# Optimization experiments

Hardware: AMD Instinct MI355X
Metric: run time of the kernel (lower is better)

Reference implementation:

```python
import jax, jax.numpy as jnp
import numpy as np

LAMBDA = 0.95   # cfg.lambda_decay
ETA = 0.5       # cfg.eta
EPS_REL = 1e-6  # cfg.epsilon (relative-error denom)
S_INNER = 3     # cfg.inner_steps
LN_EPS = 1e-5   # torch LayerNorm default eps

T, B, D_G, D_H = 48, 48, 256, 512


def setup_inputs() -> dict:
    key = jax.random.key(0)
    ks = jax.random.split(key, 5)
    # scale weights ~ kaiming/xavier so the recurrence is well-behaved
    return {
        "z_seq": jax.random.normal(ks[0], (T, B, D_G), jnp.float32),
        "clean_vec": jax.random.normal(ks[1], (B, D_G), jnp.float32),
        "W_h": jax.random.normal(ks[2], (D_H, D_H), jnp.float32) * (2.0 / D_H) ** 0.5,
        "W_g": jax.random.normal(ks[3], (D_H, D_G), jnp.float32) * (1.0 / D_G) ** 0.5,
        "b_h": jnp.zeros((D_H,), jnp.float32),
        "gamma": jnp.ones((D_H,), jnp.float32),
        "beta": jnp.zeros((D_H,), jnp.float32),
        "W_head": jax.random.normal(ks[4], (D_G, D_H), jnp.float32) * (1.0 / D_H) ** 0.5,
        "b_head": jnp.zeros((D_G,), jnp.float32),
    }


def _layernorm(x, gamma, beta):
    mu = jnp.mean(x, axis=-1, keepdims=True)
    var = jnp.mean(jnp.square(x - mu), axis=-1, keepdims=True)
    return (x - mu) * jax.lax.rsqrt(var + LN_EPS) * gamma + beta


def reference(z_seq, clean_vec, W_h, W_g, b_h, gamma, beta, W_head, b_head):
    Bsz = clean_vec.shape[0]
    d_h = W_h.shape[0]
    h0 = jnp.zeros((Bsz, d_h), z_seq.dtype)
    A0 = jnp.zeros((Bsz, d_h, d_h), z_seq.dtype)

    def step(carry, z_t):
        h_prev, A = carry
        base = h_prev @ W_h.T + z_t @ W_g.T + b_h          # (B, d_h)
        h = jax.nn.relu(_layernorm(base, gamma, beta))
        for _ in range(S_INNER):                            # inner fast-weight settling
            add_Ah = jnp.einsum('bij,bj->bi', A, h)         # bmm(A, h)
            h = jax.nn.relu(_layernorm(base + add_Ah, gamma, beta))
        A = LAMBDA * A + ETA * jnp.einsum('bi,bj->bij', h, h)  # Hebbian outer-product update
        return (h, A), None

    (h, A), _ = jax.lax.scan(step, (h0, A0), z_seq)

    pred_vec = h @ W_head.T + b_head                        # (B, d_g)
    pred_norm = pred_vec / (jnp.linalg.norm(pred_vec, axis=1, keepdims=True) + 1e-6)
    clean_norm = clean_vec / (jnp.linalg.norm(clean_vec, axis=1, keepdims=True) + 1e-6)
    sq_err = jnp.sum(jnp.square(pred_vec - clean_vec), axis=1)
    denom = jnp.sum(jnp.square(clean_vec), axis=1) + EPS_REL
    loss = jnp.mean(sq_err / denom)
    acc = jnp.mean(jnp.sum(pred_norm * clean_norm, axis=1))
    return loss, acc
```

## Files before the change

### kernel.cpp

```cpp
#include <hip/hip_runtime.h>

#define T_STEPS 48
#define BATCH   48
#define DG      256
#define DH      512
#define S_INNER 3
#define HDSTRIDE 260

typedef _Float16 hf2 __attribute__((ext_vector_type(2)));

__device__ __forceinline__ hf2 bch(unsigned u) { return __builtin_bit_cast(hf2, u); }
__device__ __forceinline__ unsigned pkh(_Float16 a, _Float16 b) {
  hf2 v{a, b}; return __builtin_bit_cast(unsigned, v);
}
__device__ __forceinline__ float fdot2u(unsigned a, unsigned b, float c) {
#if __has_builtin(__builtin_amdgcn_fdot2)
  return __builtin_amdgcn_fdot2(bch(a), bch(b), c, false);
#else
  hf2 x = bch(a), y = bch(b);
  return fmaf((float)x.x, (float)y.x, fmaf((float)x.y, (float)y.y, c));
#endif
}
__device__ __forceinline__ float wave_reduce_sum(float v) {
  #pragma unroll
  for (int off = 32; off > 0; off >>= 1) v += __shfl_xor(v, off, 64);
  return v;
}
template <int CTRL>
__device__ __forceinline__ float dpp_add(float v) {
  int t = __builtin_amdgcn_update_dpp(0, __float_as_int(v), CTRL, 0xf, 0xf, true);
  return v + __int_as_float(t);
}
template <int CTRL>
__device__ __forceinline__ float dpp_mov(float v) {
  return __int_as_float(
      __builtin_amdgcn_update_dpp(0, __float_as_int(v), CTRL, 0xf, 0xf, true));
}
__device__ __forceinline__ float wave64_sum63(float v) {
  v = dpp_add<0xB1>(v);
  v = dpp_add<0x4E>(v);
  v = dpp_add<0x141>(v);
  v = dpp_add<0x140>(v);
  v = dpp_add<0x142>(v);
  v = dpp_add<0x143>(v);
  return v;
}
__device__ __forceinline__ float row16_sum(float v) {
  v = dpp_add<0xB1>(v);
  v = dpp_add<0x4E>(v);
  v = dpp_add<0x141>(v);
  v = dpp_add<0x140>(v);
  return v;
}

__global__ __launch_bounds__(256)
void pack_whq(const float* __restrict__ W, uint2* __restrict__ Wq) {
  int idx = blockIdx.x * 256 + threadIdx.x;
  int j = idx & (DH - 1), q = idx >> 9;
  float w0 = W[(size_t)(4 * q + 0) * DH + j];
  float w1 = W[(size_t)(4 * q + 1) * DH + j];
  float w2 = W[(size_t)(4 * q + 2) * DH + j];
  float w3 = W[(size_t)(4 * q + 3) * DH + j];
  uint2 o;
  o.x = pkh((_Float16)w0, (_Float16)w1);
  o.y = pkh((_Float16)w2, (_Float16)w3);
  Wq[(size_t)j * 128 + q] = o;
}

__global__ __launch_bounds__(256)
void transpose_k(const float* __restrict__ in, float* __restrict__ out, int R, int C) {
  __shared__ float tile[32][33];
  int c0 = blockIdx.x * 32, r0 = blockIdx.y * 32;
  int tx = threadIdx.x & 31, ty = threadIdx.x >> 5;
  #pragma unroll
  for (int k = 0; k < 32; k += 8)
    tile[ty + k][tx] = in[(size_t)(r0 + ty + k) * C + (c0 + tx)];
  __syncthreads();
  #pragma unroll
  for (int k = 0; k < 32; k += 8)
    out[(size_t)(c0 + ty + k) * R + (r0 + tx)] = tile[tx][ty + k];
}

__global__ __launch_bounds__(DH, 2)
void zg_kernel(const float* __restrict__ z, const float* __restrict__ WgT,
               float* __restrict__ ZG) {
  const int row0 = blockIdx.x * 8;
  const int tid = threadIdx.x;
  __shared__ __align__(16) float zl[8][DG];
  for (int i = tid; i < 8 * (DG / 4); i += DH) {
    int r = i >> 6, c = i & 63;
    ((float4*)zl[r])[c] = ((const float4*)(z + (size_t)(row0 + r) * DG))[c];
  }
  __syncthreads();
  float acc[8] = {0.f, 0.f, 0.f, 0.f, 0.f, 0.f, 0.f, 0.f};
  for (int j = 0; j < DG; j += 4) {
    float w0 = WgT[(size_t)(j + 0) * DH + tid];
    float w1 = WgT[(size_t)(j + 1) * DH + tid];
    float w2 = WgT[(size_t)(j + 2) * DH + tid];
    float w3 = WgT[(size_t)(j + 3) * DH + tid];
    #pragma unroll
    for (int r = 0; r < 8; ++r) {
      float4 zz = ((const float4*)zl[r])[j >> 2];
      acc[r] = fmaf(w0, zz.x, acc[r]);
      acc[r] = fmaf(w1, zz.y, acc[r]);
      acc[r] = fmaf(w2, zz.z, acc[r]);
      acc[r] = fmaf(w3, zz.w, acc[r]);
    }
  }
  #pragma unroll
  for (int r = 0; r < 8; ++r)
    ZG[(size_t)(row0 + r) * DH + tid] = acc[r];
}

#define HCASE(s) case (2*(s)): hreg[(s)] = hb; break; \
                 case (2*(s)+1): hreg[(s)] |= (hb << 16); break;

__global__ __launch_bounds__(1024, 4)
void rnn_main(const float* __restrict__ ZG, const uint2* __restrict__ Whq,
              const float* __restrict__ bh, const float* __restrict__ gamma,
              const float* __restrict__ beta, const float* __restrict__ W_head,
              const float* __restrict__ b_head, const float* __restrict__ clean,
              float* __restrict__ outbuf) {
  const int b = blockIdx.x;
  const int tid  = threadIdx.x;
  const int lane = tid & 63;
  const int wv   = tid >> 6;
  const int dim  = tid;
  const bool lower = tid < DH;
  const int q     = tid & 127;
  const int slice = tid >> 7;
  const bool isdot = tid < 768;
  const int dst = tid >> 4;
  const int dj  = tid & 15;

  __shared__ __align__(16) unsigned histd[T_STEPS * HDSTRIDE];
  __shared__ __align__(16) float    pm[8 * DH];
  __shared__ __align__(16) uint2    APr[8 * 64];
  __shared__ __align__(16) unsigned h2cur[256];
  __shared__ __align__(16) unsigned cbufh2[24];
  __shared__ __align__(16) float    hcur[DH];
  __shared__ __align__(16) float    pred[DG];
  __shared__ float2 red[8];
  __shared__ float  red4[64];
  __shared__ int    wcntp[8];
  __shared__ float  lampow[T_STEPS];

  float g_i = 0.f, be_i = 0.f, bh_i = 0.f;
  if (lower) { g_i = gamma[dim]; be_i = beta[dim]; bh_i = bh[dim]; }
  if (tid == 0) {
    float pw = 0.5f;
    for (int k = 0; k < T_STEPS; ++k) { lampow[k] = pw; pw *= 0.95f; }
  }
  unsigned hreg[24];
  #pragma unroll
  for (int k = 0; k < 24; ++k) hreg[k] = 0u;

  const char* Wb = (const char*)Whq;
  const unsigned q8 = (unsigned)(q << 3);
  __syncthreads();

  for (int t = 0; t < T_STEPS; ++t) {
    float zg = lower ? ZG[((size_t)t * BATCH + b) * DH + dim] : 0.f;

    uint4 hr0, hr1, hr2, hr3;
    if (isdot) {
      const unsigned* rp = histd + dst * HDSTRIDE + 4 * dj;
      hr0 = *(const uint4*)(rp + 0);
      hr1 = *(const uint4*)(rp + 64);
      hr2 = *(const uint4*)(rp + 128);
      hr3 = *(const uint4*)(rp + 192);
    } else {
      hr0 = hr1 = hr2 = hr3 = make_uint4(0u, 0u, 0u, 0u);
    }

    {
      hf2 ma0{}, ma1{}, mc0{}, mc1{};
      if (t > 0) {
        const int n = wcntp[slice];
        if (n > 0) {
          const uint4* ap4 = (const uint4*)(APr + slice * 64);
          uint4 E0 = ap4[0], E1 = ap4[1];
          uint2 w0 = *(const uint2*)(Wb + (E0.x + q8));
          uint2 w1 = *(const uint2*)(Wb + (E0.z + q8));
          uint2 w2 = *(const uint2*)(Wb + (E1.x + q8));
          uint2 w3 = *(const uint2*)(Wb + (E1.z + q8));
          for (int m = 4; m < n; m += 4) {
            uint4 F0 = ap4[m >> 1], F1 = ap4[(m >> 1) + 1];
            uint2 v0 = *(const uint2*)(Wb + (F0.x + q8));
            uint2 v1 = *(const uint2*)(Wb + (F0.z + q8));
            uint2 v2 = *(const uint2*)(Wb + (F1.x + q8));
            uint2 v3 = *(const uint2*)(Wb + (F1.z + q8));
            ma0 += bch(w0.x) * bch(E0.y); mc0 += bch(w0.y) * bch(E0.y);
            ma1 += bch(w1.x) * bch(E0.w); mc1 += bch(w1.y) * bch(E0.w);
            ma0 += bch(w2.x) * bch(E1.y); mc0 += bch(w2.y) * bch(E1.y);
            ma1 += bch(w3.x) * bch(E1.w); mc1 += bch(w3.y) * bch(E1.w);
            E0 = F0; E1 = F1;
            w0 = v0; w1 = v1; w2 = v2; w3 = v3;
          }
          ma0 += bch(w0.x) * bch(E0.y); mc0 += bch(w0.y) * bch(E0.y);
          ma1 += bch(w1.x) * bch(E0.w); mc1 += bch(w1.y) * bch(E0.w);
          ma0 += bch(w2.x) * bch(E1.y); mc0 += bch(w2.y) * bch(E1.y);
          ma1 += bch(w3.x) * bch(E1.w); mc1 += bch(w3.y) * bch(E1.w);
        }
      }
      float4 s4;
      s4.x = (float)ma0.x + (float)ma1.x; s4.y = (float)ma0.y + (float)ma1.y;
      s4.z = (float)mc0.x + (float)mc1.x; s4.w = (float)mc0.y + (float)mc1.y;
      ((float4*)(pm + slice * DH))[q] = s4;
    }
    __syncthreads();

    float base_i = 0.f;
    if (lower) {
      base_i = bh_i + zg;
      if (t > 0) {
        float ps = 0.f;
        #pragma unroll
        for (int sl = 0; sl < 8; ++sl) ps += pm[sl * DH + dim];
        base_i += ps;
      }
    }

    for (int inr = 0; inr <= S_INNER; ++inr) {
      float x = 0.f;
      if (lower) {
        float Ah = 0.f;
        if (inr > 0 && t > 0) {
          const uint4* cbp = (const uint4*)cbufh2;
          uint4 c0 = cbp[0], c1 = cbp[1], c2 = cbp[2];
          uint4 c3 = cbp[3], c4 = cbp[4], c5 = cbp[5];
          float A0 = 0.f, A1 = 0.f, A2 = 0.f, A3 = 0.f;
          A0 = fdot2u(hreg[0],  c0.x, A0); A1 = fdot2u(hreg[1],  c0.y, A1);
          A2 = fdot2u(hreg[2],  c0.z, A2); A3 = fdot2u(hreg[3],  c0.w, A3);
          A0 = fdot2u(hreg[4],  c1.x, A0); A1 = fdot2u(hreg[5],  c1.y, A1);
          A2 = fdot2u(hreg[6],  c1.z, A2); A3 = fdot2u(hreg[7],  c1.w, A3);
          A0 = fdot2u(hreg[8],  c2.x, A0); A1 = fdot2u(hreg[9],  c2.y, A1);
          A2 = fdot2u(hreg[10], c2.z, A2); A3 = fdot2u(hreg[11], c2.w, A3);
          A0 = fdot2u(hreg[12], c3.x, A0); A1 = fdot2u(hreg[13], c3.y, A1);
          A2 = fdot2u(hreg[14], c3.z, A2); A3 = fdot2u(hreg[15], c3.w, A3);
          A0 = fdot2u(hreg[16], c4.x, A0); A1 = fdot2u(hreg[17], c4.y, A1);
          A2 = fdot2u(hreg[18], c4.z, A2); A3 = fdot2u(hreg[19], c4.w, A3);
          A0 = fdot2u(hreg[20], c5.x, A0); A1 = fdot2u(hreg[21], c5.y, A1);
          A2 = fdot2u(hreg[22], c5.z, A2); A3 = fdot2u(hreg[23], c5.w, A3);
          Ah = (A0 + A1) + (A2 + A3);
        }
        x = base_i + Ah;
        float sa = wave64_sum63(x);
        float sb = wave64_sum63(x * x);
        if (lane == 63) red[wv] = make_float2(sa, sb);
      }
      __syncthreads();

      if (inr < S_INNER) {
        if (lower) {
          const float4* rr = (const float4*)red;
          float4 r0 = rr[0], r1 = rr[1], r2 = rr[2], r3 = rr[3];
          float s  = ((r0.x + r1.x) + (r2.x + r3.x)) + ((r0.z + r1.z) + (r2.z + r3.z));
          float s2 = ((r0.y + r1.y) + (r2.y + r3.y)) + ((r0.w + r1.w) + (r2.w + r3.w));
          const float inv = 1.f / (float)DH;
          float mu  = s * inv;
          float var = s2 * inv - mu * mu;
          float rstd = rsqrtf(var + 1e-5f);
          float h = fmaxf(fmaf((x - mu) * rstd, g_i, be_i), 0.f);
          float hn = dpp_mov<0xB1>(h);
          if (!(dim & 1)) h2cur[dim >> 1] = pkh((_Float16)h, (_Float16)hn);
        }
        __syncthreads();
        if (isdot) {
          const unsigned* hp = h2cur + 4 * dj;
          uint4 v0 = *(const uint4*)(hp + 0);
          uint4 v1 = *(const uint4*)(hp + 64);
          uint4 v2 = *(const uint4*)(hp + 128);
          uint4 v3 = *(const uint4*)(hp + 192);
          float a0 = 0.f, a1 = 0.f, a2 = 0.f, a3 = 0.f;
          a0 = fdot2u(hr0.x, v0.x, a0); a1 = fdot2u(hr0.y, v0.y, a1);
          a2 = fdot2u(hr0.z, v0.z, a2); a3 = fdot2u(hr0.w, v0.w, a3);
          a0 = fdot2u(hr1.x, v1.x, a0); a1 = fdot2u(hr1.y, v1.y, a1);
          a2 = fdot2u(hr1.z, v1.z, a2); a3 = fdot2u(hr1.w, v1.w, a3);
          a0 = fdot2u(hr2.x, v2.x, a0); a1 = fdot2u(hr2.y, v2.y, a1);
          a2 = fdot2u(hr2.z, v2.z, a2); a3 = fdot2u(hr2.w, v2.w, a3);
          a0 = fdot2u(hr3.x, v3.x, a0); a1 = fdot2u(hr3.y, v3.y, a1);
          a2 = fdot2u(hr3.z, v3.z, a2); a3 = fdot2u(hr3.w, v3.w, a3);
          float pd = row16_sum((a0 + a1) + (a2 + a3));
          float cc = (dst < t) ? pd * lampow[t - 1 - dst] : 0.f;
          if (dj == 0) {
            _Float16 ch = (_Float16)cc;
            ((unsigned short*)cbufh2)[dst] = __builtin_bit_cast(unsigned short, ch);
          }
        }
        __syncthreads();
      } else {
        if (lower) {
          const float4* rr = (const float4*)red;
          float4 r0 = rr[0], r1 = rr[1], r2 = rr[2], r3 = rr[3];
          float s  = ((r0.x + r1.x) + (r2.x + r3.x)) + ((r0.z + r1.z) + (r2.z + r3.z));
          float s2 = ((r0.y + r1.y) + (r2.y + r3.y)) + ((r0.w + r1.w) + (r2.w + r3.w));
          const float inv = 1.f / (float)DH;
          float mu  = s * inv;
          float var = s2 * inv - mu * mu;
          float rstd = rsqrtf(var + 1e-5f);
          float h = fmaxf(fmaf((x - mu) * rstd, g_i, be_i), 0.f);
          unsigned hb = (unsigned)__builtin_bit_cast(unsigned short, (_Float16)h);
          float hn = dpp_mov<0xB1>(h);
          if (!(dim & 1))
            histd[t * HDSTRIDE + (dim >> 1)] = pkh((_Float16)h, (_Float16)hn);
          switch (t) {
            HCASE(0)  HCASE(1)  HCASE(2)  HCASE(3)  HCASE(4)  HCASE(5)
            HCASE(6)  HCASE(7)  HCASE(8)  HCASE(9)  HCASE(10) HCASE(11)
            HCASE(12) HCASE(13) HCASE(14) HCASE(15) HCASE(16) HCASE(17)
            HCASE(18) HCASE(19) HCASE(20) HCASE(21) HCASE(22) HCASE(23)
          }
          if (t == T_STEPS - 1) hcur[dim] = h;
          unsigned long long mb = __ballot(h != 0.f);
          int myoff = __popcll(mb & ((1ull << lane) - 1ull));
          int wc  = __popcll(mb);
          int wcp = (wc + 3) & ~3;
          if (h != 0.f) {
            _Float16 hh = (_Float16)h;
            uint2 ent; ent.x = (unsigned)(dim << 10); ent.y = pkh(hh, hh);
            APr[wv * 64 + myoff] = ent;
          } else {
            int inact = lane - myoff;
            if (inact < wcp - wc) {
              uint2 zz; zz.x = 0u; zz.y = 0u;
              APr[wv * 64 + wc + inact] = zz;
            }
          }
          if (lane == 0) wcntp[wv] = wcp;
        }
        __syncthreads();
      }
    }
  }

  for (int r = wv; r < DG; r += 16) {
    const float4* w4  = (const float4*)(W_head + (size_t)r * DH);
    const float4* hc4 = (const float4*)hcur;
    float pdot = 0.f;
    #pragma unroll
    for (int kk = 0; kk < 2; ++kk) {
      float4 a4 = w4[lane + 64 * kk];
      float4 c4 = hc4[lane + 64 * kk];
      pdot += a4.x * c4.x + a4.y * c4.y + a4.z * c4.z + a4.w * c4.w;
    }
    pdot = wave_reduce_sum(pdot);
    if (lane == 0) pred[r] = pdot + b_head[r];
  }
  __syncthreads();

  float sq = 0.f, pc = 0.f, pp = 0.f, cc = 0.f;
  if (tid < DG) {
    float pv = pred[tid];
    float cv = clean[(size_t)b * DG + tid];
    float d = pv - cv;
    sq = d * d; pc = pv * cv; pp = pv * pv; cc = cv * cv;
  }
  #pragma unroll
  for (int off = 32; off > 0; off >>= 1) {
    sq += __shfl_xor(sq, off, 64);
    pc += __shfl_xor(pc, off, 64);
    pp += __shfl_xor(pp, off, 64);
    cc += __shfl_xor(cc, off, 64);
  }
  if (lane == 0) {
    red4[wv * 4 + 0] = sq; red4[wv * 4 + 1] = pc;
    red4[wv * 4 + 2] = pp; red4[wv * 4 + 3] = cc;
  }
  __syncthreads();
  if (tid == 0) {
    float Sq = 0.f, Pc = 0.f, Pp = 0.f, Cc = 0.f;
    #pragma unroll
    for (int w = 0; w < 16; ++w) {
      Sq += red4[w * 4 + 0]; Pc += red4[w * 4 + 1];
      Pp += red4[w * 4 + 2]; Cc += red4[w * 4 + 3];
    }
    outbuf[b]         = Sq / (Cc + 1e-6f);
    outbuf[BATCH + b] = Pc / ((sqrtf(Pp) + 1e-6f) * (sqrtf(Cc) + 1e-6f));
  }
}

__global__ __launch_bounds__(64)
void finalize_k(const float* __restrict__ outbuf, float* __restrict__ out) {
  int tid = threadIdx.x;
  float l = (tid < BATCH) ? outbuf[tid] : 0.f;
  float a = (tid < BATCH) ? outbuf[BATCH + tid] : 0.f;
  #pragma unroll
  for (int off = 32; off > 0; off >>= 1) {
    l += __shfl_xor(l, off, 64);
    a += __shfl_xor(a, off, 64);
  }
  if (tid == 0) {
    out[0] = l * (1.f / (float)BATCH);
    out[1] = a * (1.f / (float)BATCH);
  }
}

extern "C" void kernel_launch(void* const* d_in, const int* in_sizes, int n_in,
                              void* d_out, int out_size, void* d_ws, size_t ws_size,
                              hipStream_t stream) {
  (void)in_sizes; (void)n_in; (void)out_size; (void)ws_size;
  const float* z      = (const float*)d_in[0];
  const float* clean  = (const float*)d_in[1];
  const float* W_h    = (const float*)d_in[2];
  const float* W_g    = (const float*)d_in[3];
  const float* b_h    = (const float*)d_in[4];
  const float* gamma  = (const float*)d_in[5];
  const float* beta   = (const float*)d_in[6];
  const float* W_head = (const float*)d_in[7];
  const float* b_head = (const float*)d_in[8];

  float* wsf     = (float*)d_ws;
  uint2* Whq     = (uint2*)wsf;
  float* WgT     = wsf + 131072;
  float* ZG      = WgT + (size_t)DG * DH;
  float* outbuf  = ZG + (size_t)T_STEPS * BATCH * DH;

  hipLaunchKernelGGL(pack_whq, dim3(256), dim3(256), 0, stream, W_h, Whq);
  hipLaunchKernelGGL(transpose_k, dim3(DG / 32, DH / 32), dim3(256), 0, stream,
                     W_g, WgT, DH, DG);
  hipLaunchKernelGGL(zg_kernel, dim3((T_STEPS * BATCH) / 8), dim3(DH), 0, stream,
                     z, WgT, ZG);
  hipLaunchKernelGGL(rnn_main, dim3(BATCH), dim3(1024), 0, stream,
                     ZG, Whq, b_h, gamma, beta, W_head, b_head, clean, outbuf);
  hipLaunchKernelGGL(finalize_k, dim3(1), dim3(64), 0, stream,
                     outbuf, (float*)d_out);
}
```

Before: 306.6 us.

## Halve rnn_main block to 512 threads, giving each thread more work

The recurrent kernel now runs with 512 threads per block instead of 1024, so every thread is active. Each thread covers more of the work: the sparse W_h matvec loads uint4 (8 fp16 weights) per active entry across a wave-wide slice, and the history-dot phase handles two history rows for the first 256 threads. Active-entry padding drops from a multiple of 4 to a multiple of 2. The aim is cheaper barriers and fewer idle lanes per step, traded for more registers per thread and longer serial work per thread.

New measurement: 286.6 us. -6.5%, faster.

```diff
diff --git a/kernel.cpp b/kernel.cpp
--- a/kernel.cpp
+++ b/kernel.cpp
@@ -115,7 +115,15 @@
 #define HCASE(s) case (2*(s)): hreg[(s)] = hb; break; \
                  case (2*(s)+1): hreg[(s)] |= (hb << 16); break;
 
-__global__ __launch_bounds__(1024, 4)
+#define MVACC(E, wA, wB) do {                                        \
+    hf2 h0 = bch((E).y), h1 = bch((E).w);                            \
+    a0 += bch((wA).x) * h0; a1 += bch((wA).y) * h0;                  \
+    a2 += bch((wA).z) * h0; a3 += bch((wA).w) * h0;                  \
+    b0 += bch((wB).x) * h1; b1 += bch((wB).y) * h1;                  \
+    b2 += bch((wB).z) * h1; b3 += bch((wB).w) * h1;                  \
+  } while (0)
+
+__global__ __launch_bounds__(512, 2)
 void rnn_main(const float* __restrict__ ZG, const uint2* __restrict__ Whq,
               const float* __restrict__ bh, const float* __restrict__ gamma,
               const float* __restrict__ beta, const float* __restrict__ W_head,
@@ -126,12 +134,9 @@
   const int lane = tid & 63;
   const int wv   = tid >> 6;
   const int dim  = tid;
-  const bool lower = tid < DH;
-  const int q     = tid & 127;
-  const int slice = tid >> 7;
-  const bool isdot = tid < 768;
-  const int dst = tid >> 4;
-  const int dj  = tid & 15;
+  const int g    = tid >> 4;
+  const int dj   = tid & 15;
+  const bool g16 = tid < 256;
 
   __shared__ __align__(16) unsigned histd[T_STEPS * HDSTRIDE];
   __shared__ __align__(16) float    pm[8 * DH];
@@ -140,13 +145,14 @@
   __shared__ __align__(16) unsigned cbufh2[24];
   __shared__ __align__(16) float    hcur[DH];
   __shared__ __align__(16) float    pred[DG];
-  __shared__ float2 red[8];
-  __shared__ float  red4[64];
+  __shared__ __align__(16) float2   red[8];
+  __shared__ float  red4[32];
   __shared__ int    wcntp[8];
   __shared__ float  lampow[T_STEPS];
 
-  float g_i = 0.f, be_i = 0.f, bh_i = 0.f;
-  if (lower) { g_i = gamma[dim]; be_i = beta[dim]; bh_i = bh[dim]; }
+  const float g_i  = gamma[dim];
+  const float be_i = beta[dim];
+  const float bh_i = bh[dim];
   if (tid == 0) {
     float pw = 0.5f;
     for (int k = 0; k < T_STEPS; ++k) { lampow[k] = pw; pw *= 0.95f; }
@@ -156,74 +162,80 @@
   for (int k = 0; k < 24; ++k) hreg[k] = 0u;
 
   const char* Wb = (const char*)Whq;
-  const unsigned q8 = (unsigned)(q << 3);
+  const unsigned l16 = (unsigned)(lane << 4);
   __syncthreads();
 
   for (int t = 0; t < T_STEPS; ++t) {
-    float zg = lower ? ZG[((size_t)t * BATCH + b) * DH + dim] : 0.f;
-
-    uint4 hr0, hr1, hr2, hr3;
-    if (isdot) {
-      const unsigned* rp = histd + dst * HDSTRIDE + 4 * dj;
-      hr0 = *(const uint4*)(rp + 0);
-      hr1 = *(const uint4*)(rp + 64);
-      hr2 = *(const uint4*)(rp + 128);
-      hr3 = *(const uint4*)(rp + 192);
-    } else {
-      hr0 = hr1 = hr2 = hr3 = make_uint4(0u, 0u, 0u, 0u);
-    }
-
+    float zg = ZG[((size_t)t * BATCH + b) * DH + dim];
+
+    uint4 hA0, hA1, hA2, hA3, hB0, hB1, hB2, hB3;
     {
-      hf2 ma0{}, ma1{}, mc0{}, mc1{};
+      const unsigned* rpA = histd + g * HDSTRIDE + 4 * dj;
+      hA0 = *(const uint4*)(rpA + 0);
+      hA1 = *(const uint4*)(rpA + 64);
+      hA2 = *(const uint4*)(rpA + 128);
+      hA3 = *(const uint4*)(rpA + 192);
+      if (g16) {
+        const unsigned* rpB = histd + (32 + g) * HDSTRIDE + 4 * dj;
+        hB0 = *(const uint4*)(rpB + 0);
+        hB1 = *(const uint4*)(rpB + 64);
+        hB2 = *(const uint4*)(rpB + 128);
+        hB3 = *(const uint4*)(rpB + 192);
+      } else {
+        hB0 = hB1 = hB2 = hB3 = make_uint4(0u, 0u, 0u, 0u);
+      }
+    }
+
+    {
+      hf2 a0{}, a1{}, a2{}, a3{}, b0{}, b1{}, b2{}, b3{};
       if (t > 0) {
-        const int n = wcntp[slice];
+        const int n = wcntp[wv];
         if (n > 0) {
-          const uint4* ap4 = (const uint4*)(APr + slice * 64);
-          uint4 E0 = ap4[0], E1 = ap4[1];
-          uint2 w0 = *(const uint2*)(Wb + (E0.x + q8));
-          uint2 w1 = *(const uint2*)(Wb + (E0.z + q8));
-          uint2 w2 = *(const uint2*)(Wb + (E1.x + q8));
-          uint2 w3 = *(const uint2*)(Wb + (E1.z + q8));
-          for (int m = 4; m < n; m += 4) {
-            uint4 F0 = ap4[m >> 1], F1 = ap4[(m >> 1) + 1];
-            uint2 v0 = *(const uint2*)(Wb + (F0.x + q8));
-            uint2 v1 = *(const uint2*)(Wb + (F0.z + q8));
-            uint2 v2 = *(const uint2*)(Wb + (F1.x + q8));
-            uint2 v3 = *(const uint2*)(Wb + (F1.z + q8));
-            ma0 += bch(w0.x) * bch(E0.y); mc0 += bch(w0.y) * bch(E0.y);
-            ma1 += bch(w1.x) * bch(E0.w); mc1 += bch(w1.y) * bch(E0.w);
-            ma0 += bch(w2.x) * bch(E1.y); mc0 += bch(w2.y) * bch(E1.y);
-            ma1 += bch(w3.x) * bch(E1.w); mc1 += bch(w3.y) * bch(E1.w);
-            E0 = F0; E1 = F1;
-            w0 = v0; w1 = v1; w2 = v2; w3 = v3;
-          }
-          ma0 += bch(w0.x) * bch(E0.y); mc0 += bch(w0.y) * bch(E0.y);
-          ma1 += bch(w1.x) * bch(E0.w); mc1 += bch(w1.y) * bch(E0.w);
-          ma0 += bch(w2.x) * bch(E1.y); mc0 += bch(w2.y) * bch(E1.y);
-          ma1 += bch(w3.x) * bch(E1.w); mc1 += bch(w3.y) * bch(E1.w);
+          const uint4* ap4 = (const uint4*)(APr + wv * 64);
+          const int G = n >> 1;
+          uint4 E0 = ap4[0];
+          uint4 wA = *(const uint4*)(Wb + (E0.x + l16));
+          uint4 wB = *(const uint4*)(Wb + (E0.z + l16));
+          uint4 E1 = E0; uint4 wC = wA, wD = wB;
+          if (G > 1) {
+            E1 = ap4[1];
+            wC = *(const uint4*)(Wb + (E1.x + l16));
+            wD = *(const uint4*)(Wb + (E1.z + l16));
+          }
+          for (int grp = 2; grp < G; ++grp) {
+            uint4 E2 = ap4[grp];
+            uint4 wE = *(const uint4*)(Wb + (E2.x + l16));
+            uint4 wF = *(const uint4*)(Wb + (E2.z + l16));
+            MVACC(E0, wA, wB);
+            E0 = E1; wA = wC; wB = wD;
+            E1 = E2; wC = wE; wD = wF;
+          }
+          MVACC(E0, wA, wB);
+          if (G > 1) MVACC(E1, wC, wD);
         }
       }
-      float4 s4;
-      s4.x = (float)ma0.x + (float)ma1.x; s4.y = (float)ma0.y + (float)ma1.y;
-      s4.z = (float)mc0.x + (float)mc1.x; s4.w = (float)mc0.y + (float)mc1.y;
-      ((float4*)(pm + slice * DH))[q] = s4;
+      float4 s0, s1;
+      s0.x = (float)a0.x + (float)b0.x; s0.y = (float)a0.y + (float)b0.y;
+      s0.z = (float)a1.x + (float)b1.x; s0.w = (float)a1.y + (float)b1.y;
+      s1.x = (float)a2.x + (float)b2.x; s1.y = (float)a2.y + (float)b2.y;
+      s1.z = (float)a3.x + (float)b3.x; s1.w = (float)a3.y + (float)b3.y;
+      float4* pmw = (float4*)(pm + wv * DH);
+      pmw[2 * lane + 0] = s0;
+      pmw[2 * lane + 1] = s1;
     }
     __syncthreads();
 
-    float base_i = 0.f;
-    if (lower) {
-      base_i = bh_i + zg;
-      if (t > 0) {
-        float ps = 0.f;
-        #pragma unroll
-        for (int sl = 0; sl < 8; ++sl) ps += pm[sl * DH + dim];
-        base_i += ps;
-      }
+    float base_i = bh_i + zg;
+    if (t > 0) {
+      float ps = 0.f;
+      #pragma unroll
+      for (int sl = 0; sl < 8; ++sl) ps += pm[sl * DH + dim];
+      base_i += ps;
     }
 
     for (int inr = 0; inr <= S_INNER; ++inr) {
-      float x = 0.f;
-      if (lower) {
+      float x;
+      {
         float Ah = 0.f;
         if (inr > 0 && t > 0) {
           const uint4* cbp = (const uint4*)cbufh2;
@@ -250,55 +262,69 @@
         if (lane == 63) red[wv] = make_float2(sa, sb);
       }
       __syncthreads();
+      float mu, rstd;
+      {
+        const float4* rr = (const float4*)red;
+        float4 r0 = rr[0], r1 = rr[1], r2 = rr[2], r3 = rr[3];
+        float s  = ((r0.x + r1.x) + (r2.x + r3.x)) + ((r0.z + r1.z) + (r2.z + r3.z));
+        float s2 = ((r0.y + r1.y) + (r2.y + r3.y)) + ((r0.w + r1.w) + (r2.w + r3.w));
+        const float inv = 1.f / (float)DH;
+        mu = s * inv;
+        float var = s2 * inv - mu * mu;
+        rstd = rsqrtf(var + 1e-5f);
+      }
 
       if (inr < S_INNER) {
-        if (lower) {
-          const float4* rr = (const float4*)red;
-          float4 r0 = rr[0], r1 = rr[1], r2 = rr[2], r3 = rr[3];
-          float s  = ((r0.x + r1.x) + (r2.x + r3.x)) + ((r0.z + r1.z) + (r2.z + r3.z));
-          float s2 = ((r0.y + r1.y) + (r2.y + r3.y)) + ((r0.w + r1.w) + (r2.w + r3.w));
-          const float inv = 1.f / (float)DH;
-          float mu  = s * inv;
-          float var = s2 * inv - mu * mu;
-          float rstd = rsqrtf(var + 1e-5f);
+        {
           float h = fmaxf(fmaf((x - mu) * rstd, g_i, be_i), 0.f);
           float hn = dpp_mov<0xB1>(h);
           if (!(dim & 1)) h2cur[dim >> 1] = pkh((_Float16)h, (_Float16)hn);
         }
         __syncthreads();
-        if (isdot) {
+        {
           const unsigned* hp = h2cur + 4 * dj;
           uint4 v0 = *(const uint4*)(hp + 0);
           uint4 v1 = *(const uint4*)(hp + 64);
           uint4 v2 = *(const uint4*)(hp + 128);
           uint4 v3 = *(const uint4*)(hp + 192);
           float a0 = 0.f, a1 = 0.f, a2 = 0.f, a3 = 0.f;
-          a0 = fdot2u(hr0.x, v0.x, a0); a1 = fdot2u(hr0.y, v0.y, a1);
-          a2 = fdot2u(hr0.z, v0.z, a2); a3 = fdot2u(hr0.w, v0.w, a3);
-          a0 = fdot2u(hr1.x, v1.x, a0); a1 = fdot2u(hr1.y, v1.y, a1);
-          a2 = fdot2u(hr1.z, v1.z, a2); a3 = fdot2u(hr1.w, v1.w, a3);
-          a0 = fdot2u(hr2.x, v2.x, a0); a1 = fdot2u(hr2.y, v2.y, a1);
-          a2 = fdot2u(hr2.z, v2.z, a2); a3 = fdot2u(hr2.w, v2.w, a3);
-          a0 = fdot2u(hr3.x, v3.x, a0); a1 = fdot2u(hr3.y, v3.y, a1);
-          a2 = fdot2u(hr3.z, v3.z, a2); a3 = fdot2u(hr3.w, v3.w, a3);
-          float pd = row16_sum((a0 + a1) + (a2 + a3));
-          float cc = (dst < t) ? pd * lampow[t - 1 - dst] : 0.f;
+          a0 = fdot2u(hA0.x, v0.x, a0); a1 = fdot2u(hA0.y, v0.y, a1);
+          a2 = fdot2u(hA0.z, v0.z, a2); a3 = fdot2u(hA0.w, v0.w, a3);
+          a0 = fdot2u(hA1.x, v1.x, a0); a1 = fdot2u(hA1.y, v1.y, a1);
+          a2 = fdot2u(hA1.z, v1.z, a2); a3 = fdot2u(hA1.w, v1.w, a3);
+          a0 = fdot2u(hA2.x, v2.x, a0); a1 = fdot2u(hA2.y, v2.y, a1);
+          a2 = fdot2u(hA2.z, v2.z, a2); a3 = fdot2u(hA2.w, v2.w, a3);
+          a0 = fdot2u(hA3.x, v3.x, a0); a1 = fdot2u(hA3.y, v3.y, a1);
+          a2 = fdot2u(hA3.z, v3.z, a2); a3 = fdot2u(hA3.w, v3.w, a3);
+          float pA = row16_sum((a0 + a1) + (a2 + a3));
+          float pB = 0.f;
+          if (g16) {
+            float e0 = 0.f, e1 = 0.f, e2 = 0.f, e3 = 0.f;
+            e0 = fdot2u(hB0.x, v0.x, e0); e1 = fdot2u(hB0.y, v0.y, e1);
+            e2 = fdot2u(hB0.z, v0.z, e2); e3 = fdot2u(hB0.w, v0.w, e3);
+            e0 = fdot2u(hB1.x, v1.x, e0); e1 = fdot2u(hB1.y, v1.y, e1);
+            e2 = fdot2u(hB1.z, v1.z, e2); e3 = fdot2u(hB1.w, v1.w, e3);
+            e0 = fdot2u(hB2.x, v2.x, e0); e1 = fdot2u(hB2.y, v2.y, e1);
+            e2 = fdot2u(hB2.z, v2.z, e2); e3 = fdot2u(hB2.w, v2.w, e3);
+            e0 = fdot2u(hB3.x, v3.x, e0); e1 = fdot2u(hB3.y, v3.y, e1);
+            e2 = fdot2u(hB3.z, v3.z, e2); e3 = fdot2u(hB3.w, v3.w, e3);
+            pB = row16_sum((e0 + e1) + (e2 + e3));
+          }
           if (dj == 0) {
-            _Float16 ch = (_Float16)cc;
-            ((unsigned short*)cbufh2)[dst] = __builtin_bit_cast(unsigned short, ch);
+            float ccA = (g < t) ? pA * lampow[t - 1 - g] : 0.f;
+            _Float16 chA = (_Float16)ccA;
+            ((unsigned short*)cbufh2)[g] = __builtin_bit_cast(unsigned short, chA);
+            if (g16) {
+              int rB = 32 + g;
+              float ccB = (rB < t) ? pB * lampow[t - 1 - rB] : 0.f;
+              _Float16 chB = (_Float16)ccB;
+              ((unsigned short*)cbufh2)[rB] = __builtin_bit_cast(unsigned short, chB);
+            }
           }
         }
         __syncthreads();
       } else {
-        if (lower) {
-          const float4* rr = (const float4*)red;
-          float4 r0 = rr[0], r1 = rr[1], r2 = rr[2], r3 = rr[3];
-          float s  = ((r0.x + r1.x) + (r2.x + r3.x)) + ((r0.z + r1.z) + (r2.z + r3.z));
-          float s2 = ((r0.y + r1.y) + (r2.y + r3.y)) + ((r0.w + r1.w) + (r2.w + r3.w));
-          const float inv = 1.f / (float)DH;
-          float mu  = s * inv;
-          float var = s2 * inv - mu * mu;
-          float rstd = rsqrtf(var + 1e-5f);
+        {
           float h = fmaxf(fmaf((x - mu) * rstd, g_i, be_i), 0.f);
           unsigned hb = (unsigned)__builtin_bit_cast(unsigned short, (_Float16)h);
           float hn = dpp_mov<0xB1>(h);
@@ -314,7 +340,7 @@
           unsigned long long mb = __ballot(h != 0.f);
           int myoff = __popcll(mb & ((1ull << lane) - 1ull));
           int wc  = __popcll(mb);
-          int wcp = (wc + 3) & ~3;
+          int wcp = (wc + 1) & ~1;
           if (h != 0.f) {
             _Float16 hh = (_Float16)h;
             uint2 ent; ent.x = (unsigned)(dim << 10); ent.y = pkh(hh, hh);
@@ -333,18 +359,15 @@
     }
   }
 
-  for (int r = wv; r < DG; r += 16) {
+  for (int r = wv; r < DG; r += 8) {
     const float4* w4  = (const float4*)(W_head + (size_t)r * DH);
     const float4* hc4 = (const float4*)hcur;
-    float pdot = 0.f;
-    #pragma unroll
-    for (int kk = 0; kk < 2; ++kk) {
-      float4 a4 = w4[lane + 64 * kk];
-      float4 c4 = hc4[lane + 64 * kk];
-      pdot += a4.x * c4.x + a4.y * c4.y + a4.z * c4.z + a4.w * c4.w;
-    }
-    pdot = wave_reduce_sum(pdot);
-    if (lane == 0) pred[r] = pdot + b_head[r];
+    float4 a4 = w4[lane];      float4 c4 = hc4[lane];
+    float4 a5 = w4[lane + 64]; float4 c5 = hc4[lane + 64];
+    float pdot = a4.x * c4.x + a4.y * c4.y + a4.z * c4.z + a4.w * c4.w
+               + a5.x * c5.x + a5.y * c5.y + a5.z * c5.z + a5.w * c5.w;
+    pdot = wave64_sum63(pdot);
+    if (lane == 63) pred[r] = pdot + b_head[r];
   }
   __syncthreads();
 
@@ -370,7 +393,7 @@
   if (tid == 0) {
     float Sq = 0.f, Pc = 0.f, Pp = 0.f, Cc = 0.f;
     #pragma unroll
-    for (int w = 0; w < 16; ++w) {
+    for (int w = 0; w < 8; ++w) {
       Sq += red4[w * 4 + 0]; Pc += red4[w * 4 + 1];
       Pp += red4[w * 4 + 2]; Cc += red4[w * 4 + 3];
     }
@@ -420,7 +443,7 @@
                      W_g, WgT, DH, DG);
   hipLaunchKernelGGL(zg_kernel, dim3((T_STEPS * BATCH) / 8), dim3(DH), 0, stream,
                      z, WgT, ZG);
-  hipLaunchKernelGGL(rnn_main, dim3(BATCH), dim3(1024), 0, stream,
+  hipLaunchKernelGGL(rnn_main, dim3(BATCH), dim3(512), 0, stream,
                      ZG, Whq, b_h, gamma, beta, W_head, b_head, clean, outbuf);
   hipLaunchKernelGGL(finalize_k, dim3(1), dim3(64), 0, stream,
                      outbuf, (float*)d_out);
```
